# Kernel optimization log

Measured on AMD Instinct MI355X. Metric: run time of the kernel, lower is better.

The kernel has to match this reference:

```python
import jax, jax.numpy as jnp
import numpy as np

H = 16  # n_heads

def _rmsnorm(x, g, eps=1e-6):
    return x * jax.lax.rsqrt(jnp.mean(x * x, axis=-1, keepdims=True) + eps) * g

def _rope_diag(L, hd, dtype):
    # Diagonal of the full [L, hd, hd] rotary matrix: cos(pos * theta_pair) at every dim.
    # (The torch einsum 'bhld,ldd->bhld' extracts this diagonal, so no pairwise rotation occurs.)
    pair = jnp.arange(hd) // 2
    theta = 10000.0 ** (-2.0 * pair / hd)
    return jnp.cos(jnp.arange(L)[:, None].astype(jnp.float32) * theta[None, :]).astype(dtype)


def setup_inputs() -> dict:
    key = jax.random.key(0)
    ks = jax.random.split(key, 8)
    B, L, E = 2, 2048, 2048
    F = 2 * E  # SwiGLU width
    s = 0.02
    return {
        "x": jax.random.normal(ks[0], (B, L, E), jnp.float32),
        "g": jnp.ones((E,), jnp.float32),
        "wq": jax.random.normal(ks[1], (E, E), jnp.float32) * s,
        "wk": jax.random.normal(ks[2], (E, E), jnp.float32) * s,
        "wv": jax.random.normal(ks[3], (E, E), jnp.float32) * s,
        "w1": jax.random.normal(ks[4], (E, F), jnp.float32) * s,
        "b1": jnp.zeros((F,), jnp.float32),
        "wg": jax.random.normal(ks[5], (F, F), jnp.float32) * s,
        "bg": jnp.zeros((F,), jnp.float32),
        "wl": jax.random.normal(ks[6], (F, F), jnp.float32) * s,
        "bl": jnp.zeros((F,), jnp.float32),
        "beta": jnp.ones((1,), jnp.float32),
        "w2": jax.random.normal(ks[7], (F, E), jnp.float32) * s,
        "b2": jnp.zeros((E,), jnp.float32),
    }


def reference(x, g, wq, wk, wv, w1, b1, wg, bg, wl, bl, beta, w2, b2):
    B, L, E = x.shape
    hd = E // H
    x_res = x
    h = _rmsnorm(x, g)
    # projections -> [B, H, L, hd]
    q = (h @ wq).reshape(B, L, H, hd).transpose(0, 2, 1, 3)
    k = (h @ wk).reshape(B, L, H, hd).transpose(0, 2, 1, 3)
    v = (h @ wv).reshape(B, L, H, hd).transpose(0, 2, 1, 3)
    D = _rope_diag(L, hd, x.dtype)  # [L, hd], diagonal of rotary matrix
    q = q * D
    k = k * D
    score = jnp.einsum('bhld,bhmd->bhlm', q, k)  # [B,H,L,L]
    # causal mask added BEFORE scaling (faithful to source)
    mask = jnp.triu(jnp.full((L, L), -jnp.inf, dtype=score.dtype), k=1)
    score = (score + mask) / jnp.sqrt(jnp.asarray(hd, score.dtype))
    attn = jax.nn.softmax(score, axis=-1)
    o = jnp.einsum('bhlm,bhmd->bhld', attn, v)
    o = o.transpose(0, 2, 1, 3).reshape(B, L, E)
    x = o + x_res
    x_res = x
    h = _rmsnorm(x, g)
    h = h @ w1 + b1  # [B, L, 2E]
    gate = h @ wg + bg
    lin = h @ wl + bl
    act = gate * jax.nn.sigmoid(beta * gate) * lin
    out = act @ w2 + b2
    return out + x_res
```

## Files before the change

### kernel.cpp

```cpp
#include <hip/hip_runtime.h>
#include <cstdint>
#include <math.h>


typedef _Float16 f16;
typedef _Float16 f16x8 __attribute__((ext_vector_type(8)));
typedef _Float16 f16x4 __attribute__((ext_vector_type(4)));
typedef float    f32x4 __attribute__((ext_vector_type(4)));

#define MFMA_16x16x32(a, b, c) __builtin_amdgcn_mfma_f32_16x16x32_f16(a, b, c, 0, 0, 0)

__device__ __forceinline__ void gload_lds16(const void* g, void* lds) {
  __builtin_amdgcn_global_load_lds(
      (__attribute__((address_space(1))) void*)(uintptr_t)g,
      (__attribute__((address_space(3))) void*)(unsigned)(uintptr_t)lds,
      16, 0, 0);
}

__global__ void convT_k(const float* __restrict__ W, f16* __restrict__ Wt,
                        int K, int N) {
  __shared__ float tile[32][33];
  const int n0 = blockIdx.x << 5, k0 = blockIdx.y << 5;
  const int t = threadIdx.x;
  const int r = t >> 3, c4 = (t & 7) << 2;
  const f32x4 v = *(const f32x4*)(W + (size_t)(k0 + r) * N + n0 + c4);
  tile[r][c4 + 0] = v[0]; tile[r][c4 + 1] = v[1];
  tile[r][c4 + 2] = v[2]; tile[r][c4 + 3] = v[3];
  __syncthreads();
  f16x4 o;
  o[0] = (f16)tile[c4 + 0][r]; o[1] = (f16)tile[c4 + 1][r];
  o[2] = (f16)tile[c4 + 2][r]; o[3] = (f16)tile[c4 + 3][r];
  *(f16x4*)(Wt + (size_t)(n0 + r) * K + k0 + c4) = o;
}

__global__ void rope_tab_k(float* __restrict__ Dt) {
  const int l = blockIdx.x, d = threadIdx.x;
  const float th = __expf(-0.0719557841f * (float)(d & ~1));
  Dt[(l << 7) + d] = cosf((float)l * th);
}

__global__ void rmsnorm_k(const float* __restrict__ X, const float* __restrict__ G,
                          f16* __restrict__ H) {
  __shared__ float red[4];
  const int row = blockIdx.x, t = threadIdx.x;
  const float* xp = X + ((size_t)row << 11) + (t << 3);
  const f32x4 v0 = *(const f32x4*)xp;
  const f32x4 v1 = *(const f32x4*)(xp + 4);
  float ss = v0[0]*v0[0] + v0[1]*v0[1] + v0[2]*v0[2] + v0[3]*v0[3]
           + v1[0]*v1[0] + v1[1]*v1[1] + v1[2]*v1[2] + v1[3]*v1[3];
#pragma unroll
  for (int m = 1; m < 64; m <<= 1) ss += __shfl_xor(ss, m);
  if ((t & 63) == 0) red[t >> 6] = ss;
  __syncthreads();
  const float tot = red[0] + red[1] + red[2] + red[3];
  const float rs = rsqrtf(tot * (1.f / 2048.f) + 1e-6f);
  const float* gp = G + (t << 3);
  const f32x4 g0 = *(const f32x4*)gp, g1 = *(const f32x4*)(gp + 4);
  f16x8 o;
  o[0] = (f16)(v0[0]*rs*g0[0]); o[1] = (f16)(v0[1]*rs*g0[1]);
  o[2] = (f16)(v0[2]*rs*g0[2]); o[3] = (f16)(v0[3]*rs*g0[3]);
  o[4] = (f16)(v1[0]*rs*g1[0]); o[5] = (f16)(v1[1]*rs*g1[1]);
  o[6] = (f16)(v1[2]*rs*g1[2]); o[7] = (f16)(v1[3]*rs*g1[3]);
  *(f16x8*)(H + ((size_t)row << 11) + (t << 3)) = o;
}

__global__ void rmsnorm_h_k(const f16* __restrict__ X, const float* __restrict__ G,
                            f16* __restrict__ H) {
  __shared__ float red[4];
  const int row = blockIdx.x, t = threadIdx.x;
  const f16x8 v = *(const f16x8*)(X + ((size_t)row << 11) + (t << 3));
  float f[8];
#pragma unroll
  for (int i = 0; i < 8; ++i) f[i] = (float)v[i];
  float ss = 0.f;
#pragma unroll
  for (int i = 0; i < 8; ++i) ss += f[i] * f[i];
#pragma unroll
  for (int m = 1; m < 64; m <<= 1) ss += __shfl_xor(ss, m);
  if ((t & 63) == 0) red[t >> 6] = ss;
  __syncthreads();
  const float tot = red[0] + red[1] + red[2] + red[3];
  const float rs = rsqrtf(tot * (1.f / 2048.f) + 1e-6f);
  const float* gp = G + (t << 3);
  const f32x4 g0 = *(const f32x4*)gp, g1 = *(const f32x4*)(gp + 4);
  f16x8 o;
#pragma unroll
  for (int i = 0; i < 4; ++i) o[i] = (f16)(f[i] * rs * g0[i]);
#pragma unroll
  for (int i = 0; i < 4; ++i) o[4 + i] = (f16)(f[4 + i] * rs * g1[i]);
  *(f16x8*)(H + ((size_t)row << 11) + (t << 3)) = o;
}

__global__ void vtrans_k(const f16* __restrict__ V, f16* __restrict__ Vt) {
  __shared__ f16 tile[32][36];
  const int l0 = blockIdx.x << 5, d0 = blockIdx.y << 5, bh = blockIdx.z;
  const int b = bh >> 4, h = bh & 15;
  const int t = threadIdx.x;
  const int r = t >> 3, c4 = (t & 7) << 2;
  const f16x4 v = *(const f16x4*)(V + (size_t)((b << 11) + l0 + r) * 2048 + (h << 7) + d0 + c4);
  tile[r][c4 + 0] = v[0]; tile[r][c4 + 1] = v[1];
  tile[r][c4 + 2] = v[2]; tile[r][c4 + 3] = v[3];
  __syncthreads();
  f16x4 o;
  o[0] = tile[c4 + 0][r]; o[1] = tile[c4 + 1][r];
  o[2] = tile[c4 + 2][r]; o[3] = tile[c4 + 3][r];
  *(f16x4*)(Vt + (size_t)((bh << 7) + d0 + r) * 2048 + l0 + c4) = o;
}

template <int EPI>
__launch_bounds__(512, 2)
__global__ void gemm256_k(const f16* __restrict__ A, const f16* __restrict__ Bt,
                          void* __restrict__ Cout, int M, int N, int K,
                          const float* __restrict__ bias,
                          const f16* __restrict__ auxh,
                          const float* __restrict__ betap) {
  __shared__ alignas(16) f16 lds[65536];
  const int t = threadIdx.x, lane = t & 63, w = t >> 6;
  const int wm = w >> 2, wn = w & 3;
  const int bm = blockIdx.y << 8, bn = blockIdx.x << 8;
  const int lh = lane & 15, lq = lane >> 4;
  const int NT = K >> 6;
  const int lrow = lane >> 3;
  const int lco  = ((lane & 7) ^ lrow) << 3;

  const f16* Agl = A  + (size_t)(bm + lrow) * K + lco;
  const f16* Bgl = Bt + (size_t)(bn + lrow) * K + lco;
  const int aw = w << 3;
  const int bw = w << 4;

  f32x4 acc[8][4] = {};
  f16x8 bf[4][2];

  auto stA = [&](int tile, int half) {
    const int d = (tile & 1) << 15;
    const int k0 = tile << 6;
    const int r0 = aw + (half << 6);
    gload_lds16(Agl + (size_t)r0 * K + k0, (void*)&lds[d + r0 * 64]);
    gload_lds16(Agl + (size_t)(r0 + 128) * K + k0, (void*)&lds[d + (r0 + 128) * 64]);
  };
  auto stB = [&](int tile, int half) {
    const int d = ((tile & 1) << 15) + 16384;
    const int k0 = tile << 6;
    const int r0 = bw + (half << 7);
    gload_lds16(Bgl + (size_t)r0 * K + k0, (void*)&lds[d + r0 * 64]);
    gload_lds16(Bgl + (size_t)(r0 + 8) * K + k0, (void*)&lds[d + (r0 + 8) * 64]);
  };
  auto ldA = [&](int d, int mi, int kk) {
    const int r = (wm << 7) + (mi << 4) + lh;
    return *(const f16x8*)&lds[(d << 15) + r * 64 + ((((kk << 2) + lq) ^ (lh & 7)) << 3)];
  };
  auto ldB = [&](int d, int ni, int kk) {
    const int r = (wn << 6) + (ni << 4) + lh;
    return *(const f16x8*)&lds[(d << 15) + 16384 + r * 64 + ((((kk << 2) + lq) ^ (lh & 7)) << 3)];
  };

  stB(0, 0); stB(0, 1); stA(0, 0); stA(0, 1);
  stB(1, 0); stB(1, 1); stA(1, 0);
  asm volatile("s_waitcnt vmcnt(6)" ::: "memory");
  __builtin_amdgcn_s_barrier();

  for (int tt = 0; tt < NT; tt += 2) {
    const bool pf = (tt + 2 < NT);
#pragma unroll
    for (int hf = 0; hf < 2; ++hf) {
#pragma unroll
      for (int ph = 0; ph < 4; ++ph) {
        f16x8 a0k0 = ldA(hf, 2 * ph, 0),     a0k1 = ldA(hf, 2 * ph, 1);
        f16x8 a1k0 = ldA(hf, 2 * ph + 1, 0), a1k1 = ldA(hf, 2 * ph + 1, 1);
        if (ph == 0) {
#pragma unroll
          for (int ni = 0; ni < 4; ++ni) {
            bf[ni][0] = ldB(hf, ni, 0); bf[ni][1] = ldB(hf, ni, 1);
          }
        }
        if (hf == 0) {
          if (ph == 0) stA(tt + 1, 1);
          else if (ph == 1) { if (pf) stB(tt + 2, 0); }
          else if (ph == 2) { if (pf) stB(tt + 2, 1); }
          else              { if (pf) stA(tt + 2, 0); }
        } else {
          if (ph == 0)      { if (pf) stA(tt + 2, 1); }
          else if (ph == 1) { if (pf) stB(tt + 3, 0); }
          else if (ph == 2) { if (pf) stB(tt + 3, 1); }
          else              { if (pf) stA(tt + 3, 0); }
        }
        __builtin_amdgcn_s_barrier();
        __builtin_amdgcn_s_setprio(1);
#pragma unroll
        for (int ni = 0; ni < 4; ++ni) {
          acc[2 * ph][ni]     = MFMA_16x16x32(a0k0, bf[ni][0], acc[2 * ph][ni]);
          acc[2 * ph][ni]     = MFMA_16x16x32(a0k1, bf[ni][1], acc[2 * ph][ni]);
          acc[2 * ph + 1][ni] = MFMA_16x16x32(a1k0, bf[ni][0], acc[2 * ph + 1][ni]);
          acc[2 * ph + 1][ni] = MFMA_16x16x32(a1k1, bf[ni][1], acc[2 * ph + 1][ni]);
        }
        __builtin_amdgcn_s_setprio(0);
        if (ph == 3) {
          if (hf == 0) {
            if (pf) asm volatile("s_waitcnt vmcnt(6)" ::: "memory");
            else    asm volatile("s_waitcnt vmcnt(0)" ::: "memory");
          } else if (pf) {
            asm volatile("s_waitcnt vmcnt(6)" ::: "memory");
          }
        }
        __builtin_amdgcn_s_barrier();
      }
    }
  }

  const float be = (EPI == 3) ? betap[0] : 0.f;
#pragma unroll
  for (int mi = 0; mi < 8; ++mi) {
#pragma unroll
    for (int ni = 0; ni < 4; ++ni) {
#pragma unroll
      for (int r = 0; r < 4; ++r) {
        const int grow = bm + (wm << 7) + (mi << 4) + (lq << 2) + r;
        const int gcol = bn + (wn << 6) + (ni << 4) + lh;
        float v = acc[mi][ni][r] + bias[gcol];
        const size_t off = (size_t)grow * N + gcol;
        if (EPI == 2) {
          ((f16*)Cout)[off] = (f16)v;
        } else if (EPI == 3) {
          ((f16*)Cout)[off] = (f16)(v / (1.f + __expf(-be * v)));
        } else {
          ((f16*)Cout)[off] = (f16)(v * (float)auxh[off]);
        }
      }
    }
  }
}

template <int EPI>
__launch_bounds__(256, 3)
__global__ void gemm_k(const f16* __restrict__ A, const f16* __restrict__ Bt,
                       void* __restrict__ Cout, int M, int N, int K,
                       const float* __restrict__ bias,
                       const float* __restrict__ auxf,
                       const f16* __restrict__ auxh,
                       float scale) {
  __shared__ alignas(16) f16 As[128 * 64];
  __shared__ alignas(16) f16 Bs[128 * 64];
  const int t = threadIdx.x;
  const int lane = t & 63;
  const int w = t >> 6;
  const int wm = w >> 1, wn = w & 1;
  const int bm = blockIdx.y << 7;
  const int bn = blockIdx.x << 7;
  const int lh = lane & 15, lq = lane >> 4;

  f32x4 acc[4][4] = {};

  for (int k0 = 0; k0 < K; k0 += 64) {
    __syncthreads();
#pragma unroll
    for (int i = 0; i < 4; ++i) {
      const int idx = i * 256 + (w << 6) + lane;
      const int row = idx >> 3, c = idx & 7;
      const int cs = (c ^ (row & 7)) << 3;
      gload_lds16(A + (size_t)(bm + row) * K + k0 + cs,
                  &As[(i * 256 + (w << 6)) << 3]);
      gload_lds16(Bt + (size_t)(bn + row) * K + k0 + cs,
                  &Bs[(i * 256 + (w << 6)) << 3]);
    }
    asm volatile("s_waitcnt vmcnt(0)" ::: "memory");
    __syncthreads();
#pragma unroll
    for (int kk = 0; kk < 2; ++kk) {
      f16x8 af[4], bfr[4];
#pragma unroll
      for (int mi = 0; mi < 4; ++mi) {
        const int r = (wm << 6) + (mi << 4) + lh;
        af[mi] = *(const f16x8*)&As[(r << 6) + ((((kk << 2) + lq) ^ (r & 7)) << 3)];
      }
#pragma unroll
      for (int ni = 0; ni < 4; ++ni) {
        const int r = (wn << 6) + (ni << 4) + lh;
        bfr[ni] = *(const f16x8*)&Bs[(r << 6) + ((((kk << 2) + lq) ^ (r & 7)) << 3)];
      }
#pragma unroll
      for (int mi = 0; mi < 4; ++mi)
#pragma unroll
        for (int ni = 0; ni < 4; ++ni)
          acc[mi][ni] = MFMA_16x16x32(af[mi], bfr[ni], acc[mi][ni]);
    }
  }

#pragma unroll
  for (int mi = 0; mi < 4; ++mi) {
#pragma unroll
    for (int ni = 0; ni < 4; ++ni) {
#pragma unroll
      for (int r = 0; r < 4; ++r) {
        const int grow = bm + (wm << 6) + (mi << 4) + (lq << 2) + r;
        const int gcol = bn + (wn << 6) + (ni << 4) + lh;
        float v = acc[mi][ni][r];
        const size_t off = (size_t)grow * N + gcol;
        if (EPI == 0) {
          v *= scale * auxf[((grow & 2047) << 7) + (gcol & 127)];
          ((f16*)Cout)[off] = (f16)v;
        } else if (EPI == 1) {
          ((f16*)Cout)[off] = (f16)v;
        } else if (EPI == 4) {
          ((f16*)Cout)[off] = (f16)((v + bias[gcol]) * (float)auxh[off]);
        } else {
          ((float*)Cout)[off] = v + bias[gcol] + (float)auxh[off];
        }
      }
    }
  }
}

__launch_bounds__(256, 2)
__global__ void attn_k(const f16* __restrict__ Q, const f16* __restrict__ Kb,
                       const f16* __restrict__ Vt, const float* __restrict__ Xres,
                       f16* __restrict__ X2, int* __restrict__ qcnt) {
  constexpr int L = 2048, E = 2048, HD = 128;
  __shared__ alignas(16) f16 Ks[2][64 * 128];
  __shared__ alignas(16) f16 Vs[128 * 64];
  __shared__ alignas(16) f16 Ps[4][32 * 72];
  __shared__ int s_item;

  const int t = threadIdx.x, lane = t & 63, w = t >> 6;
  const int lh = lane & 15, lq = lane >> 4;

  for (;;) {
    if (t == 0) s_item = atomicAdd(qcnt, 1);
    __syncthreads();
    const int item = s_item;
    if (item >= 512) return;
    const int bh = item & 31;
    const int q0 = (15 - (item >> 5)) << 7;
    const int b = bh >> 4, h = bh & 15;
    const int wrow0 = q0 + (w << 5);

    auto issueK = [&](int kv0, int buf) {
#pragma unroll
      for (int i = 0; i < 4; ++i) {
        const int idx = i * 256 + (w << 6) + lane;
        const int row = idx >> 4, c = idx & 15;
        gload_lds16(Kb + (size_t)(b * L + kv0 + row) * E + h * HD + ((c ^ (row & 7)) << 3),
                    &Ks[buf][(i * 256 + (w << 6)) << 3]);
      }
    };
    auto issueV = [&](int kv0) {
#pragma unroll
      for (int i = 0; i < 4; ++i) {
        const int idx = i * 256 + (w << 6) + lane;
        const int row = idx >> 3, c = idx & 7;
        gload_lds16(Vt + ((size_t)bh * HD + row) * L + kv0 + ((c ^ (row & 7)) << 3),
                    &Vs[(i * 256 + (w << 6)) << 3]);
      }
    };

    f16x8 qf[2][4];
#pragma unroll
    for (int mi = 0; mi < 2; ++mi) {
      const f16* qrow = Q + (size_t)(b * L + wrow0 + (mi << 4) + lh) * E + h * HD;
#pragma unroll
      for (int kq = 0; kq < 4; ++kq)
        qf[mi][kq] = *(const f16x8*)(qrow + (kq << 5) + (lq << 3));
    }
    asm volatile("s_waitcnt vmcnt(0)" ::: "memory");

    f32x4 oacc[2][8] = {};
    float mrun[2][4], lrun[2][4];
#pragma unroll
    for (int mi = 0; mi < 2; ++mi)
#pragma unroll
      for (int r = 0; r < 4; ++r) { mrun[mi][r] = -1e30f; lrun[mi][r] = 0.f; }

    const int nt = (q0 + 128) >> 6;
    issueK(0, 0);
    for (int it = 0; it < nt; ++it) {
      const int cur = it & 1;
      const int kv0 = it << 6;
      const bool more = (it + 1 < nt);
      issueV(kv0);
      if (more) {
        issueK(kv0 + 64, cur ^ 1);
        asm volatile("s_waitcnt vmcnt(8)" ::: "memory");
      } else {
        asm volatile("s_waitcnt vmcnt(4)" ::: "memory");
      }
      __builtin_amdgcn_s_barrier();

      const bool active = (kv0 <= wrow0 + 31);
      if (active) {
        f32x4 sacc[2][4] = {};
#pragma unroll
        for (int kq = 0; kq < 4; ++kq) {
          f16x8 kf[4];
#pragma unroll
          for (int ni = 0; ni < 4; ++ni) {
            const int r = (ni << 4) + lh;
            kf[ni] = *(const f16x8*)&Ks[cur][(r << 7) + ((((kq << 2) + lq) ^ (r & 7)) << 3)];
          }
#pragma unroll
          for (int mi = 0; mi < 2; ++mi)
#pragma unroll
            for (int ni = 0; ni < 4; ++ni)
              sacc[mi][ni] = MFMA_16x16x32(qf[mi][kq], kf[ni], sacc[mi][ni]);
        }
        if (kv0 + 63 > wrow0) {
#pragma unroll
          for (int mi = 0; mi < 2; ++mi)
#pragma unroll
            for (int ni = 0; ni < 4; ++ni)
#pragma unroll
              for (int r = 0; r < 4; ++r) {
                const int qr = wrow0 + (mi << 4) + (lq << 2) + r;
                const int kv = kv0 + (ni << 4) + lh;
                if (kv > qr) sacc[mi][ni][r] = -1e30f;
              }
        }
        float scl[2][4], rsum[2][4];
#pragma unroll
        for (int mi = 0; mi < 2; ++mi)
#pragma unroll
          for (int r = 0; r < 4; ++r) {
            float v = fmaxf(fmaxf(sacc[mi][0][r], sacc[mi][1][r]),
                            fmaxf(sacc[mi][2][r], sacc[mi][3][r]));
            v = fmaxf(v, __shfl_xor(v, 1));
            v = fmaxf(v, __shfl_xor(v, 2));
            v = fmaxf(v, __shfl_xor(v, 4));
            v = fmaxf(v, __shfl_xor(v, 8));
            const float mnew = fmaxf(mrun[mi][r], v);
            scl[mi][r] = __expf(mrun[mi][r] - mnew);
            mrun[mi][r] = mnew;
            rsum[mi][r] = 0.f;
          }
#pragma unroll
        for (int mi = 0; mi < 2; ++mi)
#pragma unroll
          for (int ni = 0; ni < 4; ++ni)
#pragma unroll
            for (int r = 0; r < 4; ++r) {
              const float p = __expf(sacc[mi][ni][r] - mrun[mi][r]);
              rsum[mi][r] += p;
              Ps[w][((mi << 4) + (lq << 2) + r) * 72 + (ni << 4) + lh] = (f16)p;
            }
#pragma unroll
        for (int mi = 0; mi < 2; ++mi)
#pragma unroll
          for (int r = 0; r < 4; ++r) {
            float s = rsum[mi][r];
            s += __shfl_xor(s, 1);
            s += __shfl_xor(s, 2);
            s += __shfl_xor(s, 4);
            s += __shfl_xor(s, 8);
            lrun[mi][r] = lrun[mi][r] * scl[mi][r] + s;
          }
#pragma unroll
        for (int mi = 0; mi < 2; ++mi)
#pragma unroll
          for (int nd = 0; nd < 8; ++nd)
#pragma unroll
            for (int r = 0; r < 4; ++r) oacc[mi][nd][r] *= scl[mi][r];
      }

      if (more) asm volatile("s_waitcnt vmcnt(4)" ::: "memory");
      else      asm volatile("s_waitcnt vmcnt(0)" ::: "memory");
      __builtin_amdgcn_s_barrier();

      if (active) {
#pragma unroll
        for (int kp = 0; kp < 2; ++kp) {
          f16x8 pf[2];
#pragma unroll
          for (int mi = 0; mi < 2; ++mi)
            pf[mi] = *(const f16x8*)&Ps[w][((mi << 4) + lh) * 72 + (kp << 5) + (lq << 3)];
#pragma unroll
          for (int nd = 0; nd < 8; ++nd) {
            const int r = (nd << 4) + lh;
            const f16x8 vf = *(const f16x8*)&Vs[(r << 6) + ((((kp << 2) + lq) ^ (r & 7)) << 3)];
#pragma unroll
            for (int mi = 0; mi < 2; ++mi)
              oacc[mi][nd] = MFMA_16x16x32(pf[mi], vf, oacc[mi][nd]);
          }
        }
      }
      asm volatile("" ::: "memory");
      __builtin_amdgcn_s_barrier();
    }
#pragma unroll
    for (int mi = 0; mi < 2; ++mi)
#pragma unroll
      for (int nd = 0; nd < 8; ++nd)
#pragma unroll
        for (int r = 0; r < 4; ++r) {
          const int qr = wrow0 + (mi << 4) + (lq << 2) + r;
          const size_t off = (size_t)(b * L + qr) * E + h * HD + (nd << 4) + lh;
          X2[off] = (f16)(oacc[mi][nd][r] / lrun[mi][r] + Xres[off]);
        }
  }
}

extern "C" void kernel_launch(void* const* d_in, const int* in_sizes, int n_in,
                              void* d_out, int out_size, void* d_ws, size_t ws_size,
                              hipStream_t stream) {
  const float* x    = (const float*)d_in[0];
  const float* g    = (const float*)d_in[1];
  const float* wq   = (const float*)d_in[2];
  const float* wk   = (const float*)d_in[3];
  const float* wv   = (const float*)d_in[4];
  const float* w1   = (const float*)d_in[5];
  const float* b1   = (const float*)d_in[6];
  const float* wgp  = (const float*)d_in[7];
  const float* bg   = (const float*)d_in[8];
  const float* wl   = (const float*)d_in[9];
  const float* bl   = (const float*)d_in[10];
  const float* beta = (const float*)d_in[11];
  const float* w2   = (const float*)d_in[12];
  const float* b2   = (const float*)d_in[13];

  constexpr size_t MB = 1ull << 20;
  char* ws = (char*)d_ws;
  f16*   wT   = (f16*)(ws + 0 * MB);
  int*   qcnt = (int*)(ws + 31 * MB);
  float* Dt   = (float*)(ws + 32 * MB);
  f16*   hbuf = (f16*)(ws + 33 * MB);
  f16*   qbuf = (f16*)(ws + 49 * MB);
  f16*   kbuf = (f16*)(ws + 65 * MB);
  f16*   vbuf = (f16*)(ws + 81 * MB);
  f16*   vtb  = (f16*)(ws + 97 * MB);
  f16*   x2h  = (f16*)(ws + 113 * MB);
  f16*   a1   = (f16*)(ws + 49 * MB);
  f16*   sbuf = (f16*)(ws + 81 * MB);
  f16*   act  = (f16*)(ws + 145 * MB);
  (void)ws_size; (void)n_in; (void)in_sizes; (void)out_size;

  const dim3 blk(256);
  const float qscale = 0.08838834764831845f;

  rope_tab_k<<<2048, 128, 0, stream>>>(Dt);
  rmsnorm_k<<<4096, blk, 0, stream>>>(x, g, hbuf);
  hipMemsetAsync(qcnt, 0, 4, stream);

  f16* wqT = wT;
  f16* wkT = wT + (size_t)2048 * 2048;
  f16* wvT = wT + (size_t)4096 * 2048;
  convT_k<<<dim3(64, 64), blk, 0, stream>>>(wq, wqT, 2048, 2048);
  convT_k<<<dim3(64, 64), blk, 0, stream>>>(wk, wkT, 2048, 2048);
  convT_k<<<dim3(64, 64), blk, 0, stream>>>(wv, wvT, 2048, 2048);
  gemm_k<0><<<dim3(16, 32), blk, 0, stream>>>(hbuf, wqT, qbuf, 4096, 2048, 2048,
                                              nullptr, Dt, nullptr, qscale);
  gemm_k<0><<<dim3(16, 32), blk, 0, stream>>>(hbuf, wkT, kbuf, 4096, 2048, 2048,
                                              nullptr, Dt, nullptr, 1.0f);
  gemm_k<1><<<dim3(16, 32), blk, 0, stream>>>(hbuf, wvT, vbuf, 4096, 2048, 2048,
                                              nullptr, nullptr, nullptr, 1.0f);
  vtrans_k<<<dim3(64, 4, 32), blk, 0, stream>>>(vbuf, vtb);

  attn_k<<<384, blk, 0, stream>>>(qbuf, kbuf, vtb, x, x2h, qcnt);

  rmsnorm_h_k<<<4096, blk, 0, stream>>>(x2h, g, hbuf);

  convT_k<<<dim3(128, 64), blk, 0, stream>>>(w1, wT, 2048, 4096);
  gemm256_k<2><<<dim3(16, 16), 512, 0, stream>>>(hbuf, wT, a1, 4096, 4096, 2048,
                                                 b1, nullptr, nullptr);
  convT_k<<<dim3(128, 128), blk, 0, stream>>>(wgp, wT, 4096, 4096);
  gemm256_k<3><<<dim3(16, 16), 512, 0, stream>>>(a1, wT, sbuf, 4096, 4096, 4096,
                                                 bg, nullptr, beta);
  convT_k<<<dim3(128, 128), blk, 0, stream>>>(wl, wT, 4096, 4096);
  gemm_k<4><<<dim3(32, 32), blk, 0, stream>>>(a1, wT, act, 4096, 4096, 4096,
                                              bl, nullptr, sbuf, 1.0f);
  convT_k<<<dim3(64, 128), blk, 0, stream>>>(w2, wT, 4096, 2048);
  gemm_k<5><<<dim3(16, 32), blk, 0, stream>>>(act, wT, (float*)d_out, 4096, 2048, 4096,
                                              b2, nullptr, x2h, 1.0f);
}
```

Measured before the change: 728.2 us.

## Switch 256-tile GEMM to 32x32x16 MFMA and route gated-linear GEMM through it

The 256x256 GEMM kernel now uses 32x32x16 MFMA instructions with 16-float accumulators instead of 16x16x32. That cuts the number of LDS fragment reads per MFMA and the instruction count, and the LDS swizzle and epilogue row mapping are adjusted to match. The third large FFN GEMM (the lin projection times the gate) also moves from the 128-tile kernel to this 256-tile kernel, with its EPI 4 epilogue now in gemm256_k. The epilogue writes single f16 values with a different row layout, which may hurt store coalescing.

```diff
diff --git a/kernel.cpp b/kernel.cpp
--- a/kernel.cpp
+++ b/kernel.cpp
@@ -7,8 +7,10 @@
 typedef _Float16 f16x8 __attribute__((ext_vector_type(8)));
 typedef _Float16 f16x4 __attribute__((ext_vector_type(4)));
 typedef float    f32x4 __attribute__((ext_vector_type(4)));
+typedef float    f32x16 __attribute__((ext_vector_type(16)));
 
 #define MFMA_16x16x32(a, b, c) __builtin_amdgcn_mfma_f32_16x16x32_f16(a, b, c, 0, 0, 0)
+#define MFMA_32x32x16(a, b, c) __builtin_amdgcn_mfma_f32_32x32x16_f16(a, b, c, 0, 0, 0)
 
 __device__ __forceinline__ void gload_lds16(const void* g, void* lds) {
   __builtin_amdgcn_global_load_lds(
@@ -118,7 +120,7 @@
   const int t = threadIdx.x, lane = t & 63, w = t >> 6;
   const int wm = w >> 2, wn = w & 3;
   const int bm = blockIdx.y << 8, bn = blockIdx.x << 8;
-  const int lh = lane & 15, lq = lane >> 4;
+  const int l5 = lane & 31, hi = lane >> 5;
   const int NT = K >> 6;
   const int lrow = lane >> 3;
   const int lco  = ((lane & 7) ^ lrow) << 3;
@@ -128,8 +130,8 @@
   const int aw = w << 3;
   const int bw = w << 4;
 
-  f32x4 acc[8][4] = {};
-  f16x8 bf[4][2];
+  f32x16 acc[4][2] = {};
+  f16x8 bf[2][4];
 
   auto stA = [&](int tile, int half) {
     const int d = (tile & 1) << 15;
@@ -145,13 +147,13 @@
     gload_lds16(Bgl + (size_t)r0 * K + k0, (void*)&lds[d + r0 * 64]);
     gload_lds16(Bgl + (size_t)(r0 + 8) * K + k0, (void*)&lds[d + (r0 + 8) * 64]);
   };
-  auto ldA = [&](int d, int mi, int kk) {
-    const int r = (wm << 7) + (mi << 4) + lh;
-    return *(const f16x8*)&lds[(d << 15) + r * 64 + ((((kk << 2) + lq) ^ (lh & 7)) << 3)];
+  auto ldA = [&](int d, int mi, int ks) {
+    const int r = (wm << 7) + (mi << 5) + l5;
+    return *(const f16x8*)&lds[(d << 15) + r * 64 + ((((ks << 1) + hi) ^ (r & 7)) << 3)];
   };
-  auto ldB = [&](int d, int ni, int kk) {
-    const int r = (wn << 6) + (ni << 4) + lh;
-    return *(const f16x8*)&lds[(d << 15) + 16384 + r * 64 + ((((kk << 2) + lq) ^ (lh & 7)) << 3)];
+  auto ldB = [&](int d, int ni, int ks) {
+    const int r = (wn << 6) + (ni << 5) + l5;
+    return *(const f16x8*)&lds[(d << 15) + 16384 + r * 64 + ((((ks << 1) + hi) ^ (r & 7)) << 3)];
   };
 
   stB(0, 0); stB(0, 1); stA(0, 0); stA(0, 1);
@@ -165,13 +167,13 @@
     for (int hf = 0; hf < 2; ++hf) {
 #pragma unroll
       for (int ph = 0; ph < 4; ++ph) {
-        f16x8 a0k0 = ldA(hf, 2 * ph, 0),     a0k1 = ldA(hf, 2 * ph, 1);
-        f16x8 a1k0 = ldA(hf, 2 * ph + 1, 0), a1k1 = ldA(hf, 2 * ph + 1, 1);
+        f16x8 af0 = ldA(hf, ph, 0), af1 = ldA(hf, ph, 1);
+        f16x8 af2 = ldA(hf, ph, 2), af3 = ldA(hf, ph, 3);
         if (ph == 0) {
 #pragma unroll
-          for (int ni = 0; ni < 4; ++ni) {
-            bf[ni][0] = ldB(hf, ni, 0); bf[ni][1] = ldB(hf, ni, 1);
-          }
+          for (int ni = 0; ni < 2; ++ni)
+#pragma unroll
+            for (int ks = 0; ks < 4; ++ks) bf[ni][ks] = ldB(hf, ni, ks);
         }
         if (hf == 0) {
           if (ph == 0) stA(tt + 1, 1);
@@ -187,11 +189,11 @@
         __builtin_amdgcn_s_barrier();
         __builtin_amdgcn_s_setprio(1);
 #pragma unroll
-        for (int ni = 0; ni < 4; ++ni) {
-          acc[2 * ph][ni]     = MFMA_16x16x32(a0k0, bf[ni][0], acc[2 * ph][ni]);
-          acc[2 * ph][ni]     = MFMA_16x16x32(a0k1, bf[ni][1], acc[2 * ph][ni]);
-          acc[2 * ph + 1][ni] = MFMA_16x16x32(a1k0, bf[ni][0], acc[2 * ph + 1][ni]);
-          acc[2 * ph + 1][ni] = MFMA_16x16x32(a1k1, bf[ni][1], acc[2 * ph + 1][ni]);
+        for (int ni = 0; ni < 2; ++ni) {
+          acc[ph][ni] = MFMA_32x32x16(af0, bf[ni][0], acc[ph][ni]);
+          acc[ph][ni] = MFMA_32x32x16(af1, bf[ni][1], acc[ph][ni]);
+          acc[ph][ni] = MFMA_32x32x16(af2, bf[ni][2], acc[ph][ni]);
+          acc[ph][ni] = MFMA_32x32x16(af3, bf[ni][3], acc[ph][ni]);
         }
         __builtin_amdgcn_s_setprio(0);
         if (ph == 3) {
@@ -209,13 +211,13 @@
 
   const float be = (EPI == 3) ? betap[0] : 0.f;
 #pragma unroll
-  for (int mi = 0; mi < 8; ++mi) {
-#pragma unroll
-    for (int ni = 0; ni < 4; ++ni) {
-#pragma unroll
-      for (int r = 0; r < 4; ++r) {
-        const int grow = bm + (wm << 7) + (mi << 4) + (lq << 2) + r;
-        const int gcol = bn + (wn << 6) + (ni << 4) + lh;
+  for (int mi = 0; mi < 4; ++mi) {
+#pragma unroll
+    for (int ni = 0; ni < 2; ++ni) {
+#pragma unroll
+      for (int r = 0; r < 16; ++r) {
+        const int grow = bm + (wm << 7) + (mi << 5) + (r & 3) + ((r >> 2) << 3) + (hi << 2);
+        const int gcol = bn + (wn << 6) + (ni << 5) + l5;
         float v = acc[mi][ni][r] + bias[gcol];
         const size_t off = (size_t)grow * N + gcol;
         if (EPI == 2) {
@@ -300,8 +302,6 @@
           ((f16*)Cout)[off] = (f16)v;
         } else if (EPI == 1) {
           ((f16*)Cout)[off] = (f16)v;
-        } else if (EPI == 4) {
-          ((f16*)Cout)[off] = (f16)((v + bias[gcol]) * (float)auxh[off]);
         } else {
           ((float*)Cout)[off] = v + bias[gcol] + (float)auxh[off];
         }
@@ -561,8 +561,8 @@
   gemm256_k<3><<<dim3(16, 16), 512, 0, stream>>>(a1, wT, sbuf, 4096, 4096, 4096,
                                                  bg, nullptr, beta);
   convT_k<<<dim3(128, 128), blk, 0, stream>>>(wl, wT, 4096, 4096);
-  gemm_k<4><<<dim3(32, 32), blk, 0, stream>>>(a1, wT, act, 4096, 4096, 4096,
-                                              bl, nullptr, sbuf, 1.0f);
+  gemm256_k<4><<<dim3(16, 16), 512, 0, stream>>>(a1, wT, act, 4096, 4096, 4096,
+                                                 bl, sbuf, nullptr);
   convT_k<<<dim3(64, 128), blk, 0, stream>>>(w2, wT, 4096, 2048);
   gemm_k<5><<<dim3(16, 32), blk, 0, stream>>>(act, wT, (float*)d_out, 4096, 2048, 4096,
                                               b2, nullptr, x2h, 1.0f);
```

Result: slower. 798.1 us (+9.6%).

## Fuse Q/K/V projections into one GEMM and move lin GEMM to 256-tile kernel

Applied to the files above, without the earlier changes.

The three separate Q, K and V projection GEMMs become a single N=6144 GEMM over concatenated transposed weights, with a new epilogue that routes each 2048-column segment to the q, k or v region and applies the rope scale to Q and K only. This cuts two kernel launches and lets one larger grid fill the device. The gated lin GEMM (EPI 4) also moves from the 128-tile gemm_k to the 256-tile gemm256_k, relying on gemm256_k having an EPI 4 path and taking the gate buffer through a different argument slot. The V segment lands at the old vbuf offset, so the existing transpose keeps working.

```diff
diff --git a/kernel.cpp b/kernel.cpp
--- a/kernel.cpp
+++ b/kernel.cpp
@@ -294,16 +294,17 @@
         const int grow = bm + (wm << 6) + (mi << 4) + (lq << 2) + r;
         const int gcol = bn + (wn << 6) + (ni << 4) + lh;
         float v = acc[mi][ni][r];
-        const size_t off = (size_t)grow * N + gcol;
-        if (EPI == 0) {
-          v *= scale * auxf[((grow & 2047) << 7) + (gcol & 127)];
-          ((f16*)Cout)[off] = (f16)v;
+        if (EPI == 6) {
+          const int seg = gcol >> 11, c = gcol & 2047;
+          if (seg < 2) {
+            const float f = auxf[((grow & 2047) << 7) + (c & 127)];
+            v *= (seg == 0) ? scale * f : f;
+          }
+          ((f16*)Cout)[(size_t)seg * 8388608 + ((size_t)grow << 11) + c] = (f16)v;
         } else if (EPI == 1) {
-          ((f16*)Cout)[off] = (f16)v;
-        } else if (EPI == 4) {
-          ((f16*)Cout)[off] = (f16)((v + bias[gcol]) * (float)auxh[off]);
+          ((f16*)Cout)[(size_t)grow * N + gcol] = (f16)v;
         } else {
-          ((float*)Cout)[off] = v + bias[gcol] + (float)auxh[off];
+          ((float*)Cout)[(size_t)grow * N + gcol] = v + bias[gcol] + (float)auxh[(size_t)grow * N + gcol];
         }
       }
     }
@@ -519,8 +520,7 @@
   int*   qcnt = (int*)(ws + 31 * MB);
   float* Dt   = (float*)(ws + 32 * MB);
   f16*   hbuf = (f16*)(ws + 33 * MB);
-  f16*   qbuf = (f16*)(ws + 49 * MB);
-  f16*   kbuf = (f16*)(ws + 65 * MB);
+  f16*   qkv  = (f16*)(ws + 49 * MB);
   f16*   vbuf = (f16*)(ws + 81 * MB);
   f16*   vtb  = (f16*)(ws + 97 * MB);
   f16*   x2h  = (f16*)(ws + 113 * MB);
@@ -536,21 +536,14 @@
   rmsnorm_k<<<4096, blk, 0, stream>>>(x, g, hbuf);
   hipMemsetAsync(qcnt, 0, 4, stream);
 
-  f16* wqT = wT;
-  f16* wkT = wT + (size_t)2048 * 2048;
-  f16* wvT = wT + (size_t)4096 * 2048;
-  convT_k<<<dim3(64, 64), blk, 0, stream>>>(wq, wqT, 2048, 2048);
-  convT_k<<<dim3(64, 64), blk, 0, stream>>>(wk, wkT, 2048, 2048);
-  convT_k<<<dim3(64, 64), blk, 0, stream>>>(wv, wvT, 2048, 2048);
-  gemm_k<0><<<dim3(16, 32), blk, 0, stream>>>(hbuf, wqT, qbuf, 4096, 2048, 2048,
+  convT_k<<<dim3(64, 64), blk, 0, stream>>>(wq, wT, 2048, 2048);
+  convT_k<<<dim3(64, 64), blk, 0, stream>>>(wk, wT + (size_t)2048 * 2048, 2048, 2048);
+  convT_k<<<dim3(64, 64), blk, 0, stream>>>(wv, wT + (size_t)4096 * 2048, 2048, 2048);
+  gemm_k<6><<<dim3(48, 32), blk, 0, stream>>>(hbuf, wT, qkv, 4096, 6144, 2048,
                                               nullptr, Dt, nullptr, qscale);
-  gemm_k<0><<<dim3(16, 32), blk, 0, stream>>>(hbuf, wkT, kbuf, 4096, 2048, 2048,
-                                              nullptr, Dt, nullptr, 1.0f);
-  gemm_k<1><<<dim3(16, 32), blk, 0, stream>>>(hbuf, wvT, vbuf, 4096, 2048, 2048,
-                                              nullptr, nullptr, nullptr, 1.0f);
   vtrans_k<<<dim3(64, 4, 32), blk, 0, stream>>>(vbuf, vtb);
 
-  attn_k<<<384, blk, 0, stream>>>(qbuf, kbuf, vtb, x, x2h, qcnt);
+  attn_k<<<384, blk, 0, stream>>>(qkv, qkv + (size_t)8388608, vtb, x, x2h, qcnt);
 
   rmsnorm_h_k<<<4096, blk, 0, stream>>>(x2h, g, hbuf);
 
@@ -561,8 +554,8 @@
   gemm256_k<3><<<dim3(16, 16), 512, 0, stream>>>(a1, wT, sbuf, 4096, 4096, 4096,
                                                  bg, nullptr, beta);
   convT_k<<<dim3(128, 128), blk, 0, stream>>>(wl, wT, 4096, 4096);
-  gemm_k<4><<<dim3(32, 32), blk, 0, stream>>>(a1, wT, act, 4096, 4096, 4096,
-                                              bl, nullptr, sbuf, 1.0f);
+  gemm256_k<4><<<dim3(16, 16), 512, 0, stream>>>(a1, wT, act, 4096, 4096, 4096,
+                                                 bl, sbuf, nullptr);
   convT_k<<<dim3(64, 128), blk, 0, stream>>>(w2, wT, 4096, 2048);
   gemm_k<5><<<dim3(16, 32), blk, 0, stream>>>(act, wT, (float*)d_out, 4096, 2048, 4096,
                                               b2, nullptr, x2h, 1.0f);
```

After: 723.5 us. Within noise of the previous version (-0.6%).
